# Optimization experiments

Measured on AMD Instinct MI355X. Metric: run time of the kernel, lower is better.

The kernel has to match this reference:

```python
import jax, jax.numpy as jnp
import numpy as np

N_NODES = 50000
N_EDGES = 800000
IN_DIM = 100
OUT_DIM = 40
K_HOPS = 3


def setup_inputs() -> dict:
    key = jax.random.key(0)
    k1, k2, k3, k4 = jax.random.split(key, 4)
    feat = jax.random.normal(k1, (N_NODES, IN_DIM), dtype=jnp.float32)
    # fc params (PyTorch Linear default init scale ~ 1/sqrt(in_dim))
    W = jax.random.normal(k2, (OUT_DIM, IN_DIM), dtype=jnp.float32) / np.sqrt(IN_DIM)
    b = jnp.zeros((OUT_DIM,), dtype=jnp.float32)
    src = jax.random.randint(k3, (N_EDGES,), 0, N_NODES, dtype=jnp.int32)
    dst = jax.random.randint(k4, (N_EDGES,), 0, N_NODES, dtype=jnp.int32)
    return {"feat": feat, "W": W, "b": b, "src": src, "dst": dst}


def reference(feat, W, b, src, dst):
    n = feat.shape[0]
    # symmetric degree norm (DGL SGConv uses in-degrees, clamp(min=1))
    deg = jax.ops.segment_sum(jnp.ones_like(dst, dtype=feat.dtype), dst, num_segments=n)
    norm = jnp.maximum(deg, 1.0)[:, None] ** -0.5  # [N,1]
    h = feat
    for _ in range(K_HOPS):
        h = h * norm
        # SpMM: sum over incoming edges (gather src rows, scatter-add to dst)
        h = jax.ops.segment_sum(h[src], dst, num_segments=n)
        h = h * norm
    # user-supplied normalize: per-feature zero mean / unit std (unbiased std)
    h = (h - h.mean(axis=0)) / h.std(axis=0, ddof=1)
    # final linear classifier
    return h @ W.T + b
```

## Files before the change

### kernel.cpp

```cpp
#include <hip/hip_runtime.h>

#define N_NODES 50000
#define N_EDGES 800000
#define IN_DIM 100
#define OUT_DIM 40
#define ROW 50
#define ROW_PAD 64
#define SCAN_B 512
#define NSCAN_BLK ((N_NODES + SCAN_B - 1) / SCAN_B)
#define CSR_CAP (N_EDGES + N_NODES * 8 + 64)

typedef unsigned int uint;

__device__ __forceinline__ float bflo(uint u) { return __uint_as_float(u << 16); }
__device__ __forceinline__ float bfhi(uint u) { return __uint_as_float(u & 0xffff0000u); }
__device__ __forceinline__ uint packbf(float a, float b) {
    uint ua = __float_as_uint(a), ub = __float_as_uint(b);
    ua = (ua + 0x7fffu + ((ua >> 16) & 1u)) >> 16;
    ub = (ub + 0x7fffu + ((ub >> 16) & 1u)) >> 16;
    return ua | (ub << 16);
}

__global__ void zero_kernel(int* p, int n, uint* fs, uint* bufA, uint* bufB) {
    int i = blockIdx.x * blockDim.x + threadIdx.x;
    if (i < n) p[i] = 0;
    if (i < ROW_PAD) {
        fs[(size_t)N_NODES * ROW_PAD + i] = 0u;
        bufA[(size_t)N_NODES * ROW_PAD + i] = 0u;
        bufB[(size_t)N_NODES * ROW_PAD + i] = 0u;
    }
}

__global__ void deg_kernel(const int* __restrict__ dst, int* __restrict__ deg,
                           int* __restrict__ eoff) {
    int e = blockIdx.x * blockDim.x + threadIdx.x;
    if (e < N_EDGES) eoff[e] = atomicAdd(&deg[dst[e]], 1);
}

__global__ __launch_bounds__(SCAN_B) void scan1_kernel(const int* __restrict__ deg,
                                                       int* __restrict__ rowptr,
                                                       float* __restrict__ norm,
                                                       float* __restrict__ norm2,
                                                       int* __restrict__ blocksum) {
    int i = blockIdx.x * SCAN_B + threadIdx.x;
    int lane = threadIdx.x & 63, wid = threadIdx.x >> 6;
    int d = (i < N_NODES) ? deg[i] : 0;
    int da = (d + 7) & ~7;
    int v = da;
#pragma unroll
    for (int off = 1; off < 64; off <<= 1) {
        int t = __shfl_up(v, off);
        if (lane >= off) v += t;
    }
    __shared__ int wsum[8];
    if (lane == 63) wsum[wid] = v;
    __syncthreads();
    if (threadIdx.x < 8) {
        int w = wsum[threadIdx.x];
#pragma unroll
        for (int off = 1; off < 8; off <<= 1) {
            int t = __shfl_up(w, off);
            if (lane >= off) w += t;
        }
        wsum[threadIdx.x] = w;
    }
    __syncthreads();
    int woff = wid ? wsum[wid - 1] : 0;
    int incl = woff + v;
    if (i < N_NODES) {
        rowptr[i] = incl - da;
        float n1 = 1.0f / sqrtf((float)max(d, 1));
        norm[i] = n1;
        norm2[i] = n1 * n1;
    }
    if (threadIdx.x == SCAN_B - 1) blocksum[blockIdx.x] = incl;
}

__global__ __launch_bounds__(128) void scan2_kernel(const int* __restrict__ blocksum,
                                                    int* __restrict__ blockoff,
                                                    int* __restrict__ rowptr) {
    __shared__ int s[128];
    int t = threadIdx.x;
    int v = (t < NSCAN_BLK) ? blocksum[t] : 0;
    s[t] = v;
    __syncthreads();
    for (int off = 1; off < 128; off <<= 1) {
        int u = (t >= off) ? s[t - off] : 0;
        __syncthreads();
        s[t] += u;
        __syncthreads();
    }
    if (t < NSCAN_BLK) blockoff[t] = s[t] - v;
    if (t == 127) rowptr[N_NODES] = s[127];
}

__global__ __launch_bounds__(SCAN_B) void scan3_kernel(int* __restrict__ rowptr,
                                                       const int* __restrict__ blockoff,
                                                       const int* __restrict__ deg,
                                                       int* __restrict__ csr) {
    int i = blockIdx.x * SCAN_B + threadIdx.x;
    if (i < N_NODES) {
        int rp = rowptr[i] + blockoff[blockIdx.x];
        rowptr[i] = rp;
        int d = deg[i], da = (d + 7) & ~7;
        for (int k = d; k < da; ++k) csr[rp + k] = N_NODES;
    }
}

__global__ void csr_fill_kernel(const int* __restrict__ src, const int* __restrict__ dst,
                                const int* __restrict__ rowptr,
                                const int* __restrict__ eoff,
                                int* __restrict__ csr) {
    int e = blockIdx.x * blockDim.x + threadIdx.x;
    if (e < N_EDGES) csr[rowptr[dst[e]] + eoff[e]] = src[e];
}

__global__ __launch_bounds__(256) void prescale_kernel(const float* __restrict__ feat,
                                                       const float* __restrict__ norm,
                                                       uint4* __restrict__ fs4) {
    int t = blockIdx.x * 256 + threadIdx.x;
    if (t >= N_NODES * 16) return;
    int n = t >> 4, ql = t & 15;
    float nm = norm[n];
    uint4 o = make_uint4(0u, 0u, 0u, 0u);
    const float4* fr = (const float4*)(feat + (size_t)n * IN_DIM);
    if (ql < 12) {
        float4 a = fr[2 * ql], b2 = fr[2 * ql + 1];
        o.x = packbf(a.x * nm, a.y * nm);  o.y = packbf(a.z * nm, a.w * nm);
        o.z = packbf(b2.x * nm, b2.y * nm); o.w = packbf(b2.z * nm, b2.w * nm);
    } else if (ql == 12) {
        float4 a = fr[24];
        o.x = packbf(a.x * nm, a.y * nm);  o.y = packbf(a.z * nm, a.w * nm);
    }
    fs4[t] = o;
}

__global__ __launch_bounds__(128) void spmm_kernel(const uint4* __restrict__ H4,
                                                   const int* __restrict__ rowptr,
                                                   const int* __restrict__ csr,
                                                   const float* __restrict__ scale,
                                                   uint4* __restrict__ out4) {
    const int n = blockIdx.x * 2 + (threadIdx.x >> 6);
    const int l = threadIdx.x & 63;
    const int q = l >> 4;
    const int ql = l & 15;
    const int beg = rowptr[n], end = rowptr[n + 1];
    float ax0 = 0.f, ax1 = 0.f, ax2 = 0.f, ax3 = 0.f;
    float ay0 = 0.f, ay1 = 0.f, ay2 = 0.f, ay3 = 0.f;
    for (int j = beg; j < end; j += 8) {
        int s0 = csr[j + q];
        int s1 = csr[j + 4 + q];
        uint4 u0 = H4[(size_t)s0 * 16 + ql];
        uint4 u1 = H4[(size_t)s1 * 16 + ql];
        ax0 += bflo(u0.x); ay0 += bfhi(u0.x);
        ax1 += bflo(u0.y); ay1 += bfhi(u0.y);
        ax2 += bflo(u0.z); ay2 += bfhi(u0.z);
        ax3 += bflo(u0.w); ay3 += bfhi(u0.w);
        ax0 += bflo(u1.x); ay0 += bfhi(u1.x);
        ax1 += bflo(u1.y); ay1 += bfhi(u1.y);
        ax2 += bflo(u1.z); ay2 += bfhi(u1.z);
        ax3 += bflo(u1.w); ay3 += bfhi(u1.w);
    }
    ax0 += __shfl_xor(ax0, 16); ax1 += __shfl_xor(ax1, 16);
    ax2 += __shfl_xor(ax2, 16); ax3 += __shfl_xor(ax3, 16);
    ay0 += __shfl_xor(ay0, 16); ay1 += __shfl_xor(ay1, 16);
    ay2 += __shfl_xor(ay2, 16); ay3 += __shfl_xor(ay3, 16);
    ax0 += __shfl_xor(ax0, 32); ax1 += __shfl_xor(ax1, 32);
    ax2 += __shfl_xor(ax2, 32); ax3 += __shfl_xor(ax3, 32);
    ay0 += __shfl_xor(ay0, 32); ay1 += __shfl_xor(ay1, 32);
    ay2 += __shfl_xor(ay2, 32); ay3 += __shfl_xor(ay3, 32);
    if (q == 0) {
        float sc = scale[n];
        uint4 o;
        o.x = packbf(ax0 * sc, ay0 * sc);
        o.y = packbf(ax1 * sc, ay1 * sc);
        o.z = packbf(ax2 * sc, ay2 * sc);
        o.w = packbf(ax3 * sc, ay3 * sc);
        out4[(size_t)n * 16 + ql] = o;
    }
}

#define CS_BLOCKS 625
#define CS_THREADS 256
__global__ __launch_bounds__(CS_THREADS) void col_stats_kernel(const uint* __restrict__ h,
                                                               float* __restrict__ colsum,
                                                               float* __restrict__ colsq) {
    int gtid = blockIdx.x * CS_THREADS + threadIdx.x;
    const int stride = CS_BLOCKS * CS_THREADS;
    const int total = N_NODES * ROW_PAD;
    float s0 = 0.f, s1 = 0.f, q0 = 0.f, q1 = 0.f;
    for (int i = gtid; i < total; i += stride) {
        uint u = h[i];
        float a = bflo(u), b = bfhi(u);
        s0 += a; s1 += b; q0 += a * a; q1 += b * b;
    }
    __shared__ float ssum[IN_DIM], ssq[IN_DIM];
    if (threadIdx.x < IN_DIM) { ssum[threadIdx.x] = 0.f; ssq[threadIdx.x] = 0.f; }
    __syncthreads();
    int p = gtid & 63;
    if (p < ROW) {
        atomicAdd(&ssum[2 * p], s0);
        atomicAdd(&ssum[2 * p + 1], s1);
        atomicAdd(&ssq[2 * p], q0);
        atomicAdd(&ssq[2 * p + 1], q1);
    }
    __syncthreads();
    if (threadIdx.x < IN_DIM) {
        atomicAdd(&colsum[threadIdx.x], ssum[threadIdx.x]);
        atomicAdd(&colsq[threadIdx.x], ssq[threadIdx.x]);
    }
}

__global__ __launch_bounds__(256) void prep_kernel(const float* __restrict__ colsum,
                                                   const float* __restrict__ colsq,
                                                   const float* __restrict__ W,
                                                   const float* __restrict__ b,
                                                   float* __restrict__ Wt,
                                                   float* __restrict__ bp) {
    __shared__ float smean[IN_DIM];
    __shared__ float sinv[IN_DIM];
    int t = threadIdx.x;
    const float Nf = (float)N_NODES;
    if (t < IN_DIM) {
        float m = colsum[t] / Nf;
        float var = (colsq[t] - Nf * m * m) / (Nf - 1.0f);
        var = fmaxf(var, 1e-20f);
        smean[t] = m;
        sinv[t] = 1.0f / sqrtf(var);
    }
    __syncthreads();
    for (int i = t; i < IN_DIM * OUT_DIM; i += 256) {
        int o = i % OUT_DIM, f = i / OUT_DIM;
        Wt[f * OUT_DIM + o] = W[o * IN_DIM + f] * sinv[f];
    }
    if (t < OUT_DIM) {
        float acc = b[t];
        for (int f = 0; f < IN_DIM; ++f)
            acc -= smean[f] * W[t * IN_DIM + f] * sinv[f];
        bp[t] = acc;
    }
}

__global__ __launch_bounds__(256) void final_kernel(const uint4* __restrict__ h4,
                                                    const float* __restrict__ Wt,
                                                    const float* __restrict__ bp,
                                                    float* __restrict__ out) {
    __shared__ float sW[104 * OUT_DIM];
    __shared__ float sb[OUT_DIM];
    for (int i = threadIdx.x; i < 104 * OUT_DIM; i += 256)
        sW[i] = (i < IN_DIM * OUT_DIM) ? Wt[i] : 0.f;
    if (threadIdx.x < OUT_DIM) sb[threadIdx.x] = bp[threadIdx.x];
    __syncthreads();
    int t = blockIdx.x * 256 + threadIdx.x;
    if (t >= N_NODES * 10) return;
    int n = t / 10;
    int og = (t - n * 10) * 4;
    const uint4* hr = h4 + (size_t)n * 16;
    float a0 = sb[og], a1 = sb[og + 1], a2 = sb[og + 2], a3 = sb[og + 3];
#pragma unroll
    for (int r = 0; r < 13; ++r) {
        uint4 u = hr[r];
        int f = r * 8;
        float v0 = bflo(u.x), v1 = bfhi(u.x), v2 = bflo(u.y), v3 = bfhi(u.y);
        float v4 = bflo(u.z), v5 = bfhi(u.z), v6 = bflo(u.w), v7 = bfhi(u.w);
        const float* w0 = &sW[(f + 0) * OUT_DIM + og];
        const float* w1 = &sW[(f + 1) * OUT_DIM + og];
        const float* w2 = &sW[(f + 2) * OUT_DIM + og];
        const float* w3 = &sW[(f + 3) * OUT_DIM + og];
        const float* w4 = &sW[(f + 4) * OUT_DIM + og];
        const float* w5 = &sW[(f + 5) * OUT_DIM + og];
        const float* w6 = &sW[(f + 6) * OUT_DIM + og];
        const float* w7 = &sW[(f + 7) * OUT_DIM + og];
        a0 += v0 * w0[0] + v1 * w1[0] + v2 * w2[0] + v3 * w3[0]
            + v4 * w4[0] + v5 * w5[0] + v6 * w6[0] + v7 * w7[0];
        a1 += v0 * w0[1] + v1 * w1[1] + v2 * w2[1] + v3 * w3[1]
            + v4 * w4[1] + v5 * w5[1] + v6 * w6[1] + v7 * w7[1];
        a2 += v0 * w0[2] + v1 * w1[2] + v2 * w2[2] + v3 * w3[2]
            + v4 * w4[2] + v5 * w5[2] + v6 * w6[2] + v7 * w7[2];
        a3 += v0 * w0[3] + v1 * w1[3] + v2 * w2[3] + v3 * w3[3]
            + v4 * w4[3] + v5 * w5[3] + v6 * w6[3] + v7 * w7[3];
    }
    float4 o = make_float4(a0, a1, a2, a3);
    *((float4*)(out + (size_t)n * OUT_DIM + og)) = o;
}

extern "C" void kernel_launch(void* const* d_in, const int* in_sizes, int n_in,
                              void* d_out, int out_size, void* d_ws, size_t ws_size,
                              hipStream_t stream) {
    const float* feat = (const float*)d_in[0];
    const float* W    = (const float*)d_in[1];
    const float* b    = (const float*)d_in[2];
    const int*   src  = (const int*)d_in[3];
    const int*   dst  = (const int*)d_in[4];
    float* out = (float*)d_out;

    char* w = (char*)d_ws;
    int*   deg      = (int*)w;    w += N_NODES * 4;
    float* colsum   = (float*)w;  w += 128 * 4;
    float* colsq    = (float*)w;  w += 128 * 4;
    int*   eoff     = (int*)w;    w += N_EDGES * 4;
    int*   rowptr   = (int*)w;    w += 50004 * 4;
    float* norm     = (float*)w;  w += N_NODES * 4;
    float* norm2    = (float*)w;  w += N_NODES * 4;
    int*   blocksum = (int*)w;    w += 128 * 4;
    int*   blockoff = (int*)w;    w += 128 * 4;
    int*   csr      = (int*)w;    w += CSR_CAP * 4;
    float* Wt       = (float*)w;  w += IN_DIM * OUT_DIM * 4;
    float* bp       = (float*)w;  w += 64 * 4;
    w = (char*)(((size_t)w + 255) & ~(size_t)255);
    const size_t HB = (size_t)(N_NODES + 1) * ROW_PAD * 4;
    uint*  fs       = (uint*)w;   w += HB;
    uint*  bufA     = (uint*)w;   w += HB;
    uint*  bufB     = (uint*)w;   w += HB;

    {
        int nz = N_NODES + 256;
        zero_kernel<<<(nz + 255) / 256, 256, 0, stream>>>(deg, nz, fs, bufA, bufB);
    }
    deg_kernel<<<(N_EDGES + 255) / 256, 256, 0, stream>>>(dst, deg, eoff);
    scan1_kernel<<<NSCAN_BLK, SCAN_B, 0, stream>>>(deg, rowptr, norm, norm2, blocksum);
    scan2_kernel<<<1, 128, 0, stream>>>(blocksum, blockoff, rowptr);
    scan3_kernel<<<NSCAN_BLK, SCAN_B, 0, stream>>>(rowptr, blockoff, deg, csr);
    csr_fill_kernel<<<(N_EDGES + 255) / 256, 256, 0, stream>>>(src, dst, rowptr, eoff, csr);
    prescale_kernel<<<(N_NODES * 16 + 255) / 256, 256, 0, stream>>>(feat, norm, (uint4*)fs);
    spmm_kernel<<<N_NODES / 2, 128, 0, stream>>>((const uint4*)fs, rowptr, csr, norm2, (uint4*)bufA);
    spmm_kernel<<<N_NODES / 2, 128, 0, stream>>>((const uint4*)bufA, rowptr, csr, norm2, (uint4*)bufB);
    spmm_kernel<<<N_NODES / 2, 128, 0, stream>>>((const uint4*)bufB, rowptr, csr, norm, (uint4*)bufA);
    col_stats_kernel<<<CS_BLOCKS, CS_THREADS, 0, stream>>>(bufA, colsum, colsq);
    prep_kernel<<<1, 256, 0, stream>>>(colsum, colsq, W, b, Wt, bp);
    {
        int total = N_NODES * 10;
        final_kernel<<<(total + 255) / 256, 256, 0, stream>>>((const uint4*)bufA, Wt, bp, out);
    }
}
```

Baseline: 267.1 us.

## Split SpMM hops into two feature-half passes for better cache locality

The three-hop propagation is split into two independent passes, each covering half of the 64-column padded feature row (8 uint4 per node). Each half-pass gathers only 64 bytes per source row, so the working set of the gathered matrix is halved and more of it can stay in L2/MALL during random gathers. Each wavefront now processes 8 edges per iteration instead of 8 via two loads, and reduces across three shuffle levels. The cost is twice as many kernel launches and CSR index reads, plus smaller per-lane memory transactions.

```diff
diff --git a/kernel.cpp b/kernel.cpp
--- a/kernel.cpp
+++ b/kernel.cpp
@@ -135,48 +135,42 @@
     fs4[t] = o;
 }
 
-__global__ __launch_bounds__(128) void spmm_kernel(const uint4* __restrict__ H4,
-                                                   const int* __restrict__ rowptr,
-                                                   const int* __restrict__ csr,
-                                                   const float* __restrict__ scale,
-                                                   uint4* __restrict__ out4) {
+__global__ __launch_bounds__(128) void spmm_half_kernel(const uint4* __restrict__ H4,
+                                                        const int* __restrict__ rowptr,
+                                                        const int* __restrict__ csr,
+                                                        const float* __restrict__ scale,
+                                                        uint4* __restrict__ out4,
+                                                        int off4) {
     const int n = blockIdx.x * 2 + (threadIdx.x >> 6);
     const int l = threadIdx.x & 63;
-    const int q = l >> 4;
-    const int ql = l & 15;
+    const int e = l >> 3;
+    const int ql = l & 7;
     const int beg = rowptr[n], end = rowptr[n + 1];
     float ax0 = 0.f, ax1 = 0.f, ax2 = 0.f, ax3 = 0.f;
     float ay0 = 0.f, ay1 = 0.f, ay2 = 0.f, ay3 = 0.f;
     for (int j = beg; j < end; j += 8) {
-        int s0 = csr[j + q];
-        int s1 = csr[j + 4 + q];
-        uint4 u0 = H4[(size_t)s0 * 16 + ql];
-        uint4 u1 = H4[(size_t)s1 * 16 + ql];
-        ax0 += bflo(u0.x); ay0 += bfhi(u0.x);
-        ax1 += bflo(u0.y); ay1 += bfhi(u0.y);
-        ax2 += bflo(u0.z); ay2 += bfhi(u0.z);
-        ax3 += bflo(u0.w); ay3 += bfhi(u0.w);
-        ax0 += bflo(u1.x); ay0 += bfhi(u1.x);
-        ax1 += bflo(u1.y); ay1 += bfhi(u1.y);
-        ax2 += bflo(u1.z); ay2 += bfhi(u1.z);
-        ax3 += bflo(u1.w); ay3 += bfhi(u1.w);
-    }
-    ax0 += __shfl_xor(ax0, 16); ax1 += __shfl_xor(ax1, 16);
-    ax2 += __shfl_xor(ax2, 16); ax3 += __shfl_xor(ax3, 16);
-    ay0 += __shfl_xor(ay0, 16); ay1 += __shfl_xor(ay1, 16);
-    ay2 += __shfl_xor(ay2, 16); ay3 += __shfl_xor(ay3, 16);
-    ax0 += __shfl_xor(ax0, 32); ax1 += __shfl_xor(ax1, 32);
-    ax2 += __shfl_xor(ax2, 32); ax3 += __shfl_xor(ax3, 32);
-    ay0 += __shfl_xor(ay0, 32); ay1 += __shfl_xor(ay1, 32);
-    ay2 += __shfl_xor(ay2, 32); ay3 += __shfl_xor(ay3, 32);
-    if (q == 0) {
+        int s = csr[j + e];
+        uint4 u = H4[(size_t)s * 16 + off4 + ql];
+        ax0 += bflo(u.x); ay0 += bfhi(u.x);
+        ax1 += bflo(u.y); ay1 += bfhi(u.y);
+        ax2 += bflo(u.z); ay2 += bfhi(u.z);
+        ax3 += bflo(u.w); ay3 += bfhi(u.w);
+    }
+#pragma unroll
+    for (int m = 8; m <= 32; m <<= 1) {
+        ax0 += __shfl_xor(ax0, m); ax1 += __shfl_xor(ax1, m);
+        ax2 += __shfl_xor(ax2, m); ax3 += __shfl_xor(ax3, m);
+        ay0 += __shfl_xor(ay0, m); ay1 += __shfl_xor(ay1, m);
+        ay2 += __shfl_xor(ay2, m); ay3 += __shfl_xor(ay3, m);
+    }
+    if (e == 0) {
         float sc = scale[n];
         uint4 o;
         o.x = packbf(ax0 * sc, ay0 * sc);
         o.y = packbf(ax1 * sc, ay1 * sc);
         o.z = packbf(ax2 * sc, ay2 * sc);
         o.w = packbf(ax3 * sc, ay3 * sc);
-        out4[(size_t)n * 16 + ql] = o;
+        out4[(size_t)n * 16 + off4 + ql] = o;
     }
 }
 
@@ -323,9 +317,11 @@
     scan3_kernel<<<NSCAN_BLK, SCAN_B, 0, stream>>>(rowptr, blockoff, deg, csr);
     csr_fill_kernel<<<(N_EDGES + 255) / 256, 256, 0, stream>>>(src, dst, rowptr, eoff, csr);
     prescale_kernel<<<(N_NODES * 16 + 255) / 256, 256, 0, stream>>>(feat, norm, (uint4*)fs);
-    spmm_kernel<<<N_NODES / 2, 128, 0, stream>>>((const uint4*)fs, rowptr, csr, norm2, (uint4*)bufA);
-    spmm_kernel<<<N_NODES / 2, 128, 0, stream>>>((const uint4*)bufA, rowptr, csr, norm2, (uint4*)bufB);
-    spmm_kernel<<<N_NODES / 2, 128, 0, stream>>>((const uint4*)bufB, rowptr, csr, norm, (uint4*)bufA);
+    for (int off4 = 0; off4 <= 8; off4 += 8) {
+        spmm_half_kernel<<<N_NODES / 2, 128, 0, stream>>>((const uint4*)fs,   rowptr, csr, norm2, (uint4*)bufA, off4);
+        spmm_half_kernel<<<N_NODES / 2, 128, 0, stream>>>((const uint4*)bufA, rowptr, csr, norm2, (uint4*)bufB, off4);
+        spmm_half_kernel<<<N_NODES / 2, 128, 0, stream>>>((const uint4*)bufB, rowptr, csr, norm,  (uint4*)bufA, off4);
+    }
     col_stats_kernel<<<CS_BLOCKS, CS_THREADS, 0, stream>>>(bufA, colsum, colsq);
     prep_kernel<<<1, 256, 0, stream>>>(colsum, colsq, W, b, Wt, bp);
     {
```

Result: slower. 318.2 us (+19.1%).

## Assign one node per 16-lane group in SpMM with vectorized index loads

Applied to the files above, without the earlier changes.

The SpMM kernel now maps each quarter-wavefront (16 lanes) to its own destination node, so a 128-thread block handles 8 nodes instead of 2. It drops the cross-quarter shuffle reduction and instead has each group loop over its node's padded edge list. Each iteration loads eight indices with two int4 reads and issues eight row gathers. This gives more loads in flight per lane and removes the shuffle reduction. The cost is more divergence within a wavefront, since the four nodes in a wave can have different degrees, and it assumes rows are padded to multiples of 8 and aligned to 16 bytes.

```diff
diff --git a/kernel.cpp b/kernel.cpp
--- a/kernel.cpp
+++ b/kernel.cpp
@@ -140,18 +140,26 @@
                                                    const int* __restrict__ csr,
                                                    const float* __restrict__ scale,
                                                    uint4* __restrict__ out4) {
-    const int n = blockIdx.x * 2 + (threadIdx.x >> 6);
     const int l = threadIdx.x & 63;
     const int q = l >> 4;
     const int ql = l & 15;
-    const int beg = rowptr[n], end = rowptr[n + 1];
-    float ax0 = 0.f, ax1 = 0.f, ax2 = 0.f, ax3 = 0.f;
-    float ay0 = 0.f, ay1 = 0.f, ay2 = 0.f, ay3 = 0.f;
-    for (int j = beg; j < end; j += 8) {
-        int s0 = csr[j + q];
-        int s1 = csr[j + 4 + q];
-        uint4 u0 = H4[(size_t)s0 * 16 + ql];
-        uint4 u1 = H4[(size_t)s1 * 16 + ql];
+    const int n = blockIdx.x * 8 + (threadIdx.x >> 6) * 4 + q;
+    int j = rowptr[n];
+    const int e = rowptr[n + 1];
+    float ax0 = 0.f, ay0 = 0.f, ax1 = 0.f, ay1 = 0.f;
+    float ax2 = 0.f, ay2 = 0.f, ax3 = 0.f, ay3 = 0.f;
+    while (j < e) {
+        const int4* cp = (const int4*)(csr + j);
+        int4 sa = cp[0];
+        int4 sb = cp[1];
+        uint4 u0 = H4[(size_t)sa.x * 16 + ql];
+        uint4 u1 = H4[(size_t)sa.y * 16 + ql];
+        uint4 u2 = H4[(size_t)sa.z * 16 + ql];
+        uint4 u3 = H4[(size_t)sa.w * 16 + ql];
+        uint4 u4 = H4[(size_t)sb.x * 16 + ql];
+        uint4 u5 = H4[(size_t)sb.y * 16 + ql];
+        uint4 u6 = H4[(size_t)sb.z * 16 + ql];
+        uint4 u7 = H4[(size_t)sb.w * 16 + ql];
         ax0 += bflo(u0.x); ay0 += bfhi(u0.x);
         ax1 += bflo(u0.y); ay1 += bfhi(u0.y);
         ax2 += bflo(u0.z); ay2 += bfhi(u0.z);
@@ -160,24 +168,39 @@
         ax1 += bflo(u1.y); ay1 += bfhi(u1.y);
         ax2 += bflo(u1.z); ay2 += bfhi(u1.z);
         ax3 += bflo(u1.w); ay3 += bfhi(u1.w);
-    }
-    ax0 += __shfl_xor(ax0, 16); ax1 += __shfl_xor(ax1, 16);
-    ax2 += __shfl_xor(ax2, 16); ax3 += __shfl_xor(ax3, 16);
-    ay0 += __shfl_xor(ay0, 16); ay1 += __shfl_xor(ay1, 16);
-    ay2 += __shfl_xor(ay2, 16); ay3 += __shfl_xor(ay3, 16);
-    ax0 += __shfl_xor(ax0, 32); ax1 += __shfl_xor(ax1, 32);
-    ax2 += __shfl_xor(ax2, 32); ax3 += __shfl_xor(ax3, 32);
-    ay0 += __shfl_xor(ay0, 32); ay1 += __shfl_xor(ay1, 32);
-    ay2 += __shfl_xor(ay2, 32); ay3 += __shfl_xor(ay3, 32);
-    if (q == 0) {
-        float sc = scale[n];
-        uint4 o;
-        o.x = packbf(ax0 * sc, ay0 * sc);
-        o.y = packbf(ax1 * sc, ay1 * sc);
-        o.z = packbf(ax2 * sc, ay2 * sc);
-        o.w = packbf(ax3 * sc, ay3 * sc);
-        out4[(size_t)n * 16 + ql] = o;
-    }
+        ax0 += bflo(u2.x); ay0 += bfhi(u2.x);
+        ax1 += bflo(u2.y); ay1 += bfhi(u2.y);
+        ax2 += bflo(u2.z); ay2 += bfhi(u2.z);
+        ax3 += bflo(u2.w); ay3 += bfhi(u2.w);
+        ax0 += bflo(u3.x); ay0 += bfhi(u3.x);
+        ax1 += bflo(u3.y); ay1 += bfhi(u3.y);
+        ax2 += bflo(u3.z); ay2 += bfhi(u3.z);
+        ax3 += bflo(u3.w); ay3 += bfhi(u3.w);
+        ax0 += bflo(u4.x); ay0 += bfhi(u4.x);
+        ax1 += bflo(u4.y); ay1 += bfhi(u4.y);
+        ax2 += bflo(u4.z); ay2 += bfhi(u4.z);
+        ax3 += bflo(u4.w); ay3 += bfhi(u4.w);
+        ax0 += bflo(u5.x); ay0 += bfhi(u5.x);
+        ax1 += bflo(u5.y); ay1 += bfhi(u5.y);
+        ax2 += bflo(u5.z); ay2 += bfhi(u5.z);
+        ax3 += bflo(u5.w); ay3 += bfhi(u5.w);
+        ax0 += bflo(u6.x); ay0 += bfhi(u6.x);
+        ax1 += bflo(u6.y); ay1 += bfhi(u6.y);
+        ax2 += bflo(u6.z); ay2 += bfhi(u6.z);
+        ax3 += bflo(u6.w); ay3 += bfhi(u6.w);
+        ax0 += bflo(u7.x); ay0 += bfhi(u7.x);
+        ax1 += bflo(u7.y); ay1 += bfhi(u7.y);
+        ax2 += bflo(u7.z); ay2 += bfhi(u7.z);
+        ax3 += bflo(u7.w); ay3 += bfhi(u7.w);
+        j += 8;
+    }
+    float sc = scale[n];
+    uint4 o;
+    o.x = packbf(ax0 * sc, ay0 * sc);
+    o.y = packbf(ax1 * sc, ay1 * sc);
+    o.z = packbf(ax2 * sc, ay2 * sc);
+    o.w = packbf(ax3 * sc, ay3 * sc);
+    out4[(size_t)n * 16 + ql] = o;
 }
 
 #define CS_BLOCKS 625
@@ -323,9 +346,9 @@
     scan3_kernel<<<NSCAN_BLK, SCAN_B, 0, stream>>>(rowptr, blockoff, deg, csr);
     csr_fill_kernel<<<(N_EDGES + 255) / 256, 256, 0, stream>>>(src, dst, rowptr, eoff, csr);
     prescale_kernel<<<(N_NODES * 16 + 255) / 256, 256, 0, stream>>>(feat, norm, (uint4*)fs);
-    spmm_kernel<<<N_NODES / 2, 128, 0, stream>>>((const uint4*)fs, rowptr, csr, norm2, (uint4*)bufA);
-    spmm_kernel<<<N_NODES / 2, 128, 0, stream>>>((const uint4*)bufA, rowptr, csr, norm2, (uint4*)bufB);
-    spmm_kernel<<<N_NODES / 2, 128, 0, stream>>>((const uint4*)bufB, rowptr, csr, norm, (uint4*)bufA);
+    spmm_kernel<<<N_NODES / 8, 128, 0, stream>>>((const uint4*)fs, rowptr, csr, norm2, (uint4*)bufA);
+    spmm_kernel<<<N_NODES / 8, 128, 0, stream>>>((const uint4*)bufA, rowptr, csr, norm2, (uint4*)bufB);
+    spmm_kernel<<<N_NODES / 8, 128, 0, stream>>>((const uint4*)bufB, rowptr, csr, norm, (uint4*)bufA);
     col_stats_kernel<<<CS_BLOCKS, CS_THREADS, 0, stream>>>(bufA, colsum, colsq);
     prep_kernel<<<1, 256, 0, stream>>>(colsum, colsq, W, b, Wt, bp);
     {
```

New measurement: 264.4 us. No clear change (-1.0%).
